# Kernel tuning notes

Hardware: AMD Instinct MI355X
Metric: run time of the kernel (lower is better)

The kernel has to match this reference:

```python
import jax, jax.numpy as jnp
import numpy as np

B, K, V, D, L = 16, 4, 32000, 512, 32   # batch, beam, vocab, d_model, max_decode_length
ALPHA, EOS = 0.6, 2
NEG_INF = 1.0e7   # matches inf('float32') in the torch source


def setup_inputs() -> dict:
    key = jax.random.key(0)
    k1, k2, k3, k4 = jax.random.split(key, 4)
    return {
        "initial_ids": jax.random.randint(k1, (B,), 0, V, dtype=jnp.int32),
        "init_cache_h": jax.random.normal(k2, (B, D), jnp.float32),
        "embed": jax.random.normal(k3, (V, D), jnp.float32) * 0.02,
        "proj": jax.random.normal(k4, (D, V), jnp.float32) * 0.02,
    }


def _beam_search(initial_ids, init_cache_h, embed, proj):
    # initial state (padded seq of length L+1; token 0 slot holds initial ids)
    alive_seq = jnp.zeros((B, K, L + 1), jnp.int32).at[:, :, 0].set(initial_ids[:, None])
    alive_lp = jnp.tile(jnp.array([[0.0] + [-NEG_INF] * (K - 1)], jnp.float32), (B, 1))
    cache_h = jnp.broadcast_to(init_cache_h[:, None, :], (B, K, D))
    fin_seq = jnp.zeros((B, K, L + 1), jnp.int32)
    fin_sc = jnp.full((B, K), -NEG_INF, jnp.float32)
    fin_fl = jnp.zeros((B, K), bool)

    def step(state, i):
        alive_seq, alive_lp, cache_h, fin_seq, fin_sc, fin_fl = state
        # symbols_to_logits_fn: tanh-RNN LM on the last emitted token
        last = alive_seq[:, :, i]                       # [B,K] traced index -> dynamic slice
        h = jnp.tanh(cache_h + embed[last])             # [B,K,D]
        logits = jnp.einsum('bkd,dv->bkv', h, proj)     # [B,K,V]
        # log-prob combine over flattened beam*vocab, keep 2K candidates
        lp = jax.nn.log_softmax(logits, axis=-1) + alive_lp[:, :, None]
        topk_lp, topk_idx = jax.lax.top_k(lp.reshape(B, K * V), 2 * K)
        beam_idx = topk_idx // V                        # [B,2K]
        ids = topk_idx % V
        # gather beams (seq + cache) and append new token at position i+1
        topk_seq = jnp.take_along_axis(alive_seq, beam_idx[:, :, None], axis=1)
        topk_seq = topk_seq.at[:, :, i + 1].set(ids)
        new_h = jnp.take_along_axis(h, beam_idx[:, :, None], axis=1)
        new_fl = ids == EOS                             # [B,2K]
        # new alive: penalize finished, keep top K
        alive_sc = topk_lp + new_fl.astype(jnp.float32) * -NEG_INF
        n_alive_lp, top_i = jax.lax.top_k(alive_sc, K)
        n_alive_seq = jnp.take_along_axis(topk_seq, top_i[:, :, None], axis=1)
        n_cache = jnp.take_along_axis(new_h, top_i[:, :, None], axis=1)
        # new finished: length-normalized scores, merge with previous finished
        ln = ((5.0 + (i + 1).astype(jnp.float32)) / 6.0) ** ALPHA
        new_scores = topk_lp / ln + (1.0 - new_fl.astype(jnp.float32)) * -NEG_INF
        comb_seq = jnp.concatenate([fin_seq, topk_seq], axis=1)   # [B,3K,L+1]
        comb_sc = jnp.concatenate([fin_sc, new_scores], axis=1)
        comb_fl = jnp.concatenate([fin_fl, new_fl], axis=1)
        n_fin_sc, top_fi = jax.lax.top_k(comb_sc, K)
        n_fin_seq = jnp.take_along_axis(comb_seq, top_fi[:, :, None], axis=1)
        n_fin_fl = jnp.take_along_axis(comb_fl, top_fi, axis=1)
        return (n_alive_seq, n_alive_lp, n_cache, n_fin_seq, n_fin_sc, n_fin_fl), None

    state0 = (alive_seq, alive_lp, cache_h, fin_seq, fin_sc, fin_fl)
    (alive_seq, alive_lp, _, fin_seq, fin_sc, fin_fl), _ = jax.lax.scan(
        step, state0, jnp.arange(L))
    # _process_finished_state: fall back to alive beams if nothing finished
    any_fin = jnp.any(fin_fl, axis=1)
    seq = jnp.where(any_fin[:, None, None], fin_seq.astype(jnp.float32),
                    alive_seq.astype(jnp.float32))
    sc = jnp.where(any_fin[:, None], fin_sc, alive_lp)
    return seq, sc


def reference(initial_ids, init_cache_h, embed, proj):
    return _beam_search(initial_ids, init_cache_h, embed, proj)
```

## Files before the change

kernel.cpp:

```cpp
#include <hip/hip_runtime.h>
#include <math.h>

#define BB 16
#define KK 4
#define VV 32000
#define DD 512
#define LL 32
#define EOS_ID 2
#define NEGINF 1.0e7f
#define ALPHA_C 0.6f
#define NROW (BB * KK)
#define NBLK 500
#define NSLOT 8
#define SPLIT_S 2048.0f

typedef _Float16 f16x8 __attribute__((ext_vector_type(8)));
typedef float f32x4 __attribute__((ext_vector_type(4)));

#define GLOAD_LDS16(gp, lp) \
    __builtin_amdgcn_global_load_lds( \
        (const __attribute__((address_space(1))) void*)(gp), \
        (__attribute__((address_space(3))) void*)(lp), 16, 0, 0)

#define INS8(v, idx, lv, li)                                          \
    if ((v) > lv[7]) {                                                \
        bool c_[8];                                                   \
        _Pragma("unroll")                                             \
        for (int j_ = 0; j_ < 8; j_++) c_[j_] = (v) > lv[j_];         \
        _Pragma("unroll")                                             \
        for (int j_ = 7; j_ >= 1; j_--) {                             \
            lv[j_] = c_[j_] ? (c_[j_ - 1] ? lv[j_ - 1] : (v)) : lv[j_];   \
            li[j_] = c_[j_] ? (c_[j_ - 1] ? li[j_ - 1] : (idx)) : li[j_]; \
        }                                                             \
        if (c_[0]) { lv[0] = (v); li[0] = (idx); }                    \
    }

__device__ inline void pack_h(int r, int d, float v,
                              _Float16* __restrict__ hfrag_hi,
                              _Float16* __restrict__ hfrag_lo) {
    _Float16 hi = (_Float16)v;
    _Float16 lo = (_Float16)((v - (float)hi) * SPLIT_S);
    int rg = r >> 4;
    int ks = d >> 5;
    int lane = (r & 15) + 16 * ((d >> 3) & 3);
    int e = d & 7;
    int off = (((rg * 16 + ks) * 64) + lane) * 8 + e;
    hfrag_hi[off] = hi;
    hfrag_lo[off] = lo;
}

__global__ void k_init(const int* __restrict__ initial_ids,
                       int* alive_seq, float* alive_lp,
                       int* fin_seq, float* fin_sc, int* fin_fl) {
    int tid = blockIdx.x * blockDim.x + threadIdx.x;
    int nthreads = gridDim.x * blockDim.x;
    const int SEQ = NROW * (LL + 1);
    for (int idx = tid; idx < SEQ; idx += nthreads) {
        int pos = idx % (LL + 1);
        int b = (idx / (LL + 1)) / KK;
        alive_seq[idx] = (pos == 0) ? initial_ids[b] : 0;
        fin_seq[idx] = 0;
    }
    for (int idx = tid; idx < NROW; idx += nthreads) {
        int k = idx % KK;
        alive_lp[idx] = (k == 0) ? 0.0f : -NEGINF;
        fin_sc[idx] = -NEGINF;
        fin_fl[idx] = 0;
    }
}

__global__ __launch_bounds__(256) void k_bconv(const float* __restrict__ proj,
                                               _Float16* __restrict__ bfrag_hi,
                                               _Float16* __restrict__ bfrag_lo) {
    int ct = blockIdx.x;
    int t = threadIdx.x;
    int w = t >> 6, l = t & 63;
    int col = ct * 16 + (l & 15);
    int kg = l >> 4;
    for (int ks = w; ks < 16; ks += 4) {
        int k0 = ks * 32 + kg * 8;
        f16x8 hi, lo;
        #pragma unroll
        for (int j = 0; j < 8; j++) {
            float v = proj[(size_t)(k0 + j) * VV + col];
            _Float16 h = (_Float16)v;
            hi[j] = h;
            lo[j] = (_Float16)((v - (float)h) * SPLIT_S);
        }
        size_t off = (size_t)(ct * 16 + ks) * 64 + l;
        reinterpret_cast<f16x8*>(bfrag_hi)[off] = hi;
        reinterpret_cast<f16x8*>(bfrag_lo)[off] = lo;
    }
}

__global__ void k_hinit(const int* __restrict__ initial_ids,
                        const float* __restrict__ init_h,
                        const float* __restrict__ embed,
                        float* __restrict__ h_buf,
                        _Float16* __restrict__ hfrag_hi,
                        _Float16* __restrict__ hfrag_lo) {
    int row = blockIdx.x;
    int b = row >> 2;
    int t = threadIdx.x;
    int tok = initial_ids[b];
    for (int d = t; d < DD; d += 256) {
        float v = tanhf(init_h[b * DD + d] + embed[(size_t)tok * DD + d]);
        h_buf[row * DD + d] = v;
        pack_h(row, d, v, hfrag_hi, hfrag_lo);
    }
}

__global__ __launch_bounds__(256) void k_logits(
        const _Float16* __restrict__ bfrag_hi,
        const _Float16* __restrict__ bfrag_lo,
        const _Float16* __restrict__ hfrag_hi,
        const _Float16* __restrict__ hfrag_lo,
        float* __restrict__ ptv, int* __restrict__ pti,
        float* __restrict__ pm, float* __restrict__ ps) {
    int t = threadIdx.x;
    int w = t >> 6, l = t & 63;
    int ct0 = blockIdx.x * 4;
    int c0 = ct0 * 16;
    int colr = l & 15;
    int kg = l >> 4;
    int lq = l * 8;

    __shared__ _Float16 Bs[NSLOT][4][2][512];

    f16x8 ah[16], al[16];
    #pragma unroll
    for (int ks = 0; ks < 16; ks++) {
        ah[ks] = *reinterpret_cast<const f16x8*>(hfrag_hi + ((w * 16 + ks) * 64 + l) * 8);
        al[ks] = *reinterpret_cast<const f16x8*>(hfrag_lo + ((w * 16 + ks) * 64 + l) * 8);
    }
    asm volatile("s_waitcnt vmcnt(0)" ::: "memory");
    __builtin_amdgcn_sched_barrier(0);

    f32x4 acc1[4], acc2[4];
    #pragma unroll
    for (int c2 = 0; c2 < 4; c2++) {
        acc1[c2] = (f32x4){0.f, 0.f, 0.f, 0.f};
        acc2[c2] = (f32x4){0.f, 0.f, 0.f, 0.f};
    }

    auto stage = [&](int s) {
        int slot = s & 7;
        const _Float16* gh = bfrag_hi + (((size_t)(ct0 + w) * 16 + s) * 64 + l) * 8;
        const _Float16* gl = bfrag_lo + (((size_t)(ct0 + w) * 16 + s) * 64 + l) * 8;
        GLOAD_LDS16(gh, &Bs[slot][w][0][0]);
        GLOAD_LDS16(gl, &Bs[slot][w][1][0]);
    };

    stage(0); stage(1); stage(2); stage(3); stage(4); stage(5); stage(6);

#define ITER(ks, NWAIT)                                                         \
    {                                                                           \
        asm volatile("s_waitcnt vmcnt(" #NWAIT ")" ::: "memory");               \
        __builtin_amdgcn_s_barrier();                                           \
        if ((ks) + 7 < 16) stage((ks) + 7);                                     \
        f16x8 bq[4][2];                                                         \
        _Pragma("unroll")                                                       \
        for (int c2 = 0; c2 < 4; c2++) {                                        \
            bq[c2][0] = *reinterpret_cast<const f16x8*>(&Bs[(ks) & 7][c2][0][lq]); \
            bq[c2][1] = *reinterpret_cast<const f16x8*>(&Bs[(ks) & 7][c2][1][lq]); \
        }                                                                       \
        asm volatile("s_waitcnt lgkmcnt(0)" ::: "memory");                      \
        _Pragma("unroll")                                                       \
        for (int c2 = 0; c2 < 4; c2++) {                                        \
            acc1[c2] = __builtin_amdgcn_mfma_f32_16x16x32_f16(ah[(ks)], bq[c2][0], acc1[c2], 0, 0, 0); \
            acc2[c2] = __builtin_amdgcn_mfma_f32_16x16x32_f16(ah[(ks)], bq[c2][1], acc2[c2], 0, 0, 0); \
            acc2[c2] = __builtin_amdgcn_mfma_f32_16x16x32_f16(al[(ks)], bq[c2][0], acc2[c2], 0, 0, 0); \
        }                                                                       \
    }

    ITER(0, 12)  ITER(1, 12)  ITER(2, 12)  ITER(3, 12)
    ITER(4, 12)  ITER(5, 12)  ITER(6, 12)  ITER(7, 12)
    ITER(8, 12)  ITER(9, 12)  ITER(10, 10) ITER(11, 8)
    ITER(12, 6)  ITER(13, 4)  ITER(14, 2)  ITER(15, 0)
#undef ITER

    char* pool = (char*)&Bs[0][0][0][0];
    float* Cs  = (float*)pool;
    float* sv  = (float*)(pool + 16640);
    int*   si  = (int*)  (pool + 24832);
    float* smx = (float*)(pool + 33024);
    float* ssm = (float*)(pool + 34048);

    #pragma unroll
    for (int c2 = 0; c2 < 4; c2++)
        #pragma unroll
        for (int j = 0; j < 4; j++)
            Cs[(w * 16 + kg * 4 + j) * 65 + c2 * 16 + colr] =
                acc1[c2][j] + acc2[c2][j] * (1.0f / SPLIT_S);
    __syncthreads();

    int row = t >> 2, cg = t & 3;
    float lv[8]; int li[8];
    #pragma unroll
    for (int j = 0; j < 8; j++) { lv[j] = -INFINITY; li[j] = 0x7fffffff; }
    float m = -INFINITY, s = 0.0f;
    #pragma unroll
    for (int cc = 0; cc < 16; cc++) {
        float v = Cs[row * 65 + cg * 16 + cc];
        int idx = c0 + cg * 16 + cc;
        float M = fmaxf(m, v);
        s = s * expf(m - M) + expf(v - M);
        m = M;
        INS8(v, idx, lv, li)
    }
    #pragma unroll
    for (int j = 0; j < 8; j++) { sv[t * 8 + j] = lv[j]; si[t * 8 + j] = li[j]; }
    smx[t] = m; ssm[t] = s;
    __syncthreads();
    for (int st = 2; st > 0; st >>= 1) {
        if ((t & 3) < st) {
            float rv[8]; int ri[8];
            int pa = 0, pb = 0;
            #pragma unroll
            for (int j = 0; j < 8; j++) {
                bool aok = pa < 8, bok = pb < 8;
                float va = sv[t * 8 + (aok ? pa : 7)], vb = sv[(t + st) * 8 + (bok ? pb : 7)];
                int   ia = si[t * 8 + (aok ? pa : 7)], ib = si[(t + st) * 8 + (bok ? pb : 7)];
                bool takeA = !bok || (aok && ((va > vb) || (va == vb && ia <= ib)));
                if (takeA) { rv[j] = va; ri[j] = ia; pa++; }
                else       { rv[j] = vb; ri[j] = ib; pb++; }
            }
            #pragma unroll
            for (int j = 0; j < 8; j++) { sv[t * 8 + j] = rv[j]; si[t * 8 + j] = ri[j]; }
            float ma = smx[t], mb = smx[t + st];
            float M = fmaxf(ma, mb);
            ssm[t] = ssm[t] * expf(ma - M) + ssm[t + st] * expf(mb - M);
            smx[t] = M;
        }
        __syncthreads();
    }
    if ((t & 3) == 0) {
        size_t base = ((size_t)row * NBLK + blockIdx.x) * 8;
        #pragma unroll
        for (int j = 0; j < 8; j++) { ptv[base + j] = sv[t * 8 + j]; pti[base + j] = si[t * 8 + j]; }
        pm[(size_t)row * NBLK + blockIdx.x] = smx[t];
        ps[(size_t)row * NBLK + blockIdx.x] = ssm[t];
    }
}

__global__ __launch_bounds__(256) void k_merge(
        const float* __restrict__ ptv, const int* __restrict__ pti,
        const float* __restrict__ pm, const float* __restrict__ ps,
        float* __restrict__ rowtop_val, int* __restrict__ rowtop_idx,
        float* __restrict__ row_lse) {
    int row = blockIdx.x, t = threadIdx.x;
    __shared__ float sval[256][8]; __shared__ int sidx[256][8];
    __shared__ float sm[256], ss[256];
    const float* pv = ptv + (size_t)row * NBLK * 8;
    const int*   pi = pti + (size_t)row * NBLK * 8;

    #pragma unroll
    for (int j = 0; j < 8; j++) { sval[t][j] = pv[t * 8 + j]; sidx[t][j] = pi[t * 8 + j]; }
    float m = pm[(size_t)row * NBLK + t], s = ps[(size_t)row * NBLK + t];
    if (t + 256 < NBLK) {
        const float* bv = pv + (size_t)(t + 256) * 8;
        const int*   bi = pi + (size_t)(t + 256) * 8;
        float rv[8]; int ri[8];
        int pa = 0, pb = 0;
        #pragma unroll
        for (int j = 0; j < 8; j++) {
            bool aok = pa < 8, bok = pb < 8;
            float va = sval[t][aok ? pa : 7], vb = bv[bok ? pb : 7];
            int   ia = sidx[t][aok ? pa : 7], ib = bi[bok ? pb : 7];
            bool takeA = !bok || (aok && ((va > vb) || (va == vb && ia <= ib)));
            if (takeA) { rv[j] = va; ri[j] = ia; pa++; }
            else       { rv[j] = vb; ri[j] = ib; pb++; }
        }
        #pragma unroll
        for (int j = 0; j < 8; j++) { sval[t][j] = rv[j]; sidx[t][j] = ri[j]; }
        float mb = pm[(size_t)row * NBLK + t + 256], sb = ps[(size_t)row * NBLK + t + 256];
        float M = fmaxf(m, mb);
        s = s * expf(m - M) + sb * expf(mb - M);
        m = M;
    }
    sm[t] = m; ss[t] = s;
    __syncthreads();
    for (int st = 128; st > 0; st >>= 1) {
        if (t < st) {
            float rv[8]; int ri[8];
            int pa = 0, pb = 0;
            #pragma unroll
            for (int j = 0; j < 8; j++) {
                bool aok = pa < 8, bok = pb < 8;
                float va = sval[t][aok ? pa : 7], vb = sval[t + st][bok ? pb : 7];
                int   ia = sidx[t][aok ? pa : 7], ib = sidx[t + st][bok ? pb : 7];
                bool takeA = !bok || (aok && ((va > vb) || (va == vb && ia <= ib)));
                if (takeA) { rv[j] = va; ri[j] = ia; pa++; }
                else       { rv[j] = vb; ri[j] = ib; pb++; }
            }
            #pragma unroll
            for (int j = 0; j < 8; j++) { sval[t][j] = rv[j]; sidx[t][j] = ri[j]; }
            float ma = sm[t], mb = sm[t + st];
            float M = fmaxf(ma, mb);
            ss[t] = ss[t] * expf(ma - M) + ss[t + st] * expf(mb - M);
            sm[t] = M;
        }
        __syncthreads();
    }
    if (t == 0) {
        #pragma unroll
        for (int j = 0; j < 8; j++) {
            rowtop_val[row * 8 + j] = sval[0][j];
            rowtop_idx[row * 8 + j] = sidx[0][j];
        }
        row_lse[row] = sm[0] + logf(ss[0]);
    }
}

__global__ __launch_bounds__(256) void k_update(
        const float* __restrict__ embed,
        float* h_buf, int* alive_seq, float* alive_lp,
        int* fin_seq, float* fin_sc, int* fin_fl,
        const float* __restrict__ rowtop_val, const int* __restrict__ rowtop_idx,
        const float* __restrict__ row_lse,
        _Float16* __restrict__ hfrag_hi, _Float16* __restrict__ hfrag_lo,
        int step) {
    int b = blockIdx.x;
    int t = threadIdx.x;
    __shared__ float h_old[KK][DD];
    __shared__ int old_aseq[KK][LL + 1], old_fseq[KK][LL + 1];
    __shared__ float lse_s[KK], alp_s[KK];
    __shared__ float clp[32]; __shared__ int cidx[32];
    __shared__ float c_lp[8];  __shared__ int c_beam[8], c_id[8], c_fl[8];
    __shared__ float asc_s[8], comb_s[12]; __shared__ int combfl_s[12];
    __shared__ int sel_alive[KK], sel_fin[KK];
    __shared__ float n_alp[KK], n_fsc[KK]; __shared__ int n_ffl[KK];

    for (int idx = t; idx < KK * (LL + 1); idx += 256) {
        old_aseq[idx / (LL + 1)][idx % (LL + 1)] = alive_seq[b * KK * (LL + 1) + idx];
        old_fseq[idx / (LL + 1)][idx % (LL + 1)] = fin_seq[b * KK * (LL + 1) + idx];
    }
    for (int idx = t; idx < KK * DD; idx += 256)
        h_old[idx >> 9][idx & (DD - 1)] = h_buf[b * KK * DD + idx];
    if (t < KK) {
        int r = b * KK + t;
        lse_s[t] = row_lse[r];
        alp_s[t] = alive_lp[r];
    }
    __syncthreads();

    if (t < 32) {
        int row = t >> 3;
        int src = (b * KK + row) * 8 + (t & 7);
        clp[t] = rowtop_val[src] - lse_s[row] + alp_s[row];
        cidx[t] = rowtop_idx[src];
    }
    __syncthreads();
    if (t < 32) {
        int row = t >> 3;
        float mylp = clp[t];
        int mykey = row * VV + cidx[t];
        int cnt = 0;
        #pragma unroll
        for (int j = 0; j < 32; j++) {
            int kj = (j >> 3) * VV + cidx[j];
            cnt += (clp[j] > mylp) || (clp[j] == mylp && kj < mykey);
        }
        if (cnt < 8) {
            c_lp[cnt] = mylp; c_beam[cnt] = row; c_id[cnt] = cidx[t];
            c_fl[cnt] = (cidx[t] == EOS_ID) ? 1 : 0;
        }
    }
    __syncthreads();
    if (t < 8) asc_s[t] = c_lp[t] + (c_fl[t] ? -NEGINF : 0.0f);
    if (t >= 64 && t < 76) {
        int j2 = t - 64;
        if (j2 < 4) { comb_s[j2] = fin_sc[b * KK + j2]; combfl_s[j2] = fin_fl[b * KK + j2]; }
        else {
            int cc = j2 - 4;
            float ln = powf((6.0f + (float)step) / 6.0f, ALPHA_C);
            comb_s[j2] = c_lp[cc] / ln + (c_fl[cc] ? 0.0f : -NEGINF);
            combfl_s[j2] = c_fl[cc];
        }
    }
    __syncthreads();
    if (t < 8) {
        float a = asc_s[t];
        int cnt = 0;
        #pragma unroll
        for (int j = 0; j < 8; j++) cnt += (asc_s[j] > a) || (asc_s[j] == a && j < t);
        if (cnt < KK) { sel_alive[cnt] = t; n_alp[cnt] = a; }
    }
    if (t >= 64 && t < 76) {
        int j2 = t - 64;
        float cval = comb_s[j2];
        int cnt = 0;
        #pragma unroll
        for (int j = 0; j < 12; j++) cnt += (comb_s[j] > cval) || (comb_s[j] == cval && j < j2);
        if (cnt < KK) { sel_fin[cnt] = j2; n_fsc[cnt] = cval; n_ffl[cnt] = combfl_s[j2]; }
    }
    __syncthreads();

    for (int idx = t; idx < KK * (LL + 1); idx += 256) {
        int j = idx / (LL + 1), p = idx % (LL + 1);
        int cand = sel_alive[j], bm = c_beam[cand];
        alive_seq[b * KK * (LL + 1) + idx] = (p == step + 1) ? c_id[cand] : old_aseq[bm][p];
        int src = sel_fin[j];
        int fval;
        if (src < 4) fval = old_fseq[src][p];
        else {
            int c2 = src - 4, bm2 = c_beam[c2];
            fval = (p == step + 1) ? c_id[c2] : old_aseq[bm2][p];
        }
        fin_seq[b * KK * (LL + 1) + idx] = fval;
    }
    for (int idx = t; idx < KK * DD; idx += 256) {
        int j = idx >> 9, d = idx & (DD - 1);
        int cand = sel_alive[j], bm = c_beam[cand], tok = c_id[cand];
        float v = tanhf(h_old[bm][d] + embed[(size_t)tok * DD + d]);
        int r = b * KK + j;
        h_buf[(size_t)r * DD + d] = v;
        pack_h(r, d, v, hfrag_hi, hfrag_lo);
    }
    if (t < KK) {
        alive_lp[b * KK + t] = n_alp[t];
        fin_sc[b * KK + t] = n_fsc[t];
        fin_fl[b * KK + t] = n_ffl[t];
    }
}

__global__ void k_final(const int* __restrict__ alive_seq, const float* __restrict__ alive_lp,
                        const int* __restrict__ fin_seq, const float* __restrict__ fin_sc,
                        const int* __restrict__ fin_fl, float* __restrict__ out) {
    int b = blockIdx.x;
    int t = threadIdx.x;
    __shared__ int anyf;
    if (t == 0)
        anyf = fin_fl[b * KK] | fin_fl[b * KK + 1] | fin_fl[b * KK + 2] | fin_fl[b * KK + 3];
    __syncthreads();
    for (int idx = t; idx < KK * (LL + 1); idx += blockDim.x) {
        int src = anyf ? fin_seq[b * KK * (LL + 1) + idx] : alive_seq[b * KK * (LL + 1) + idx];
        out[b * KK * (LL + 1) + idx] = (float)src;
    }
    if (t < KK)
        out[BB * KK * (LL + 1) + b * KK + t] = anyf ? fin_sc[b * KK + t] : alive_lp[b * KK + t];
}

extern "C" void kernel_launch(void* const* d_in, const int* in_sizes, int n_in,
                              void* d_out, int out_size, void* d_ws, size_t ws_size,
                              hipStream_t stream) {
    const int* initial_ids = (const int*)d_in[0];
    const float* init_h = (const float*)d_in[1];
    const float* embed = (const float*)d_in[2];
    const float* proj = (const float*)d_in[3];
    float* out = (float*)d_out;

    char* ws = (char*)d_ws;
    size_t off = 0;
    auto alloc = [&](size_t bytes) -> void* {
        off = (off + 255) & ~(size_t)255;
        void* p = ws + off;
        off += bytes;
        return p;
    };
    int* alive_seq    = (int*)alloc((size_t)NROW * (LL + 1) * 4);
    int* fin_seq      = (int*)alloc((size_t)NROW * (LL + 1) * 4);
    float* alive_lp   = (float*)alloc((size_t)NROW * 4);
    float* fin_sc     = (float*)alloc((size_t)NROW * 4);
    int* fin_fl       = (int*)alloc((size_t)NROW * 4);
    float* h_buf      = (float*)alloc((size_t)NROW * DD * 4);
    float* ptv        = (float*)alloc((size_t)NROW * NBLK * 8 * 4);
    int* pti          = (int*)alloc((size_t)NROW * NBLK * 8 * 4);
    float* pm         = (float*)alloc((size_t)NROW * NBLK * 4);
    float* ps         = (float*)alloc((size_t)NROW * NBLK * 4);
    float* rowtop_val = (float*)alloc((size_t)NROW * 8 * 4);
    int* rowtop_idx   = (int*)alloc((size_t)NROW * 8 * 4);
    float* row_lse    = (float*)alloc((size_t)NROW * 4);
    _Float16* hfrag_hi = (_Float16*)alloc((size_t)NROW * DD * 2);
    _Float16* hfrag_lo = (_Float16*)alloc((size_t)NROW * DD * 2);
    _Float16* bfrag_hi = (_Float16*)alloc((size_t)VV * DD * 2);
    _Float16* bfrag_lo = (_Float16*)alloc((size_t)VV * DD * 2);

    k_init<<<16, 256, 0, stream>>>(initial_ids, alive_seq, alive_lp,
                                   fin_seq, fin_sc, fin_fl);
    k_bconv<<<2000, 256, 0, stream>>>(proj, bfrag_hi, bfrag_lo);
    k_hinit<<<NROW, 256, 0, stream>>>(initial_ids, init_h, embed, h_buf,
                                      hfrag_hi, hfrag_lo);
    for (int step = 0; step < LL; step++) {
        k_logits<<<NBLK, 256, 0, stream>>>(bfrag_hi, bfrag_lo, hfrag_hi, hfrag_lo,
                                           ptv, pti, pm, ps);
        k_merge<<<NROW, 256, 0, stream>>>(ptv, pti, pm, ps,
                                          rowtop_val, rowtop_idx, row_lse);
        k_update<<<BB, 256, 0, stream>>>(embed, h_buf, alive_seq, alive_lp,
                                         fin_seq, fin_sc, fin_fl,
                                         rowtop_val, rowtop_idx, row_lse,
                                         hfrag_hi, hfrag_lo, step);
    }
    k_final<<<BB, 64, 0, stream>>>(alive_seq, alive_lp, fin_seq, fin_sc, fin_fl, out);
}
```

Measured before the change: 1.469 ms.

## Fuse per-step logits, merge and update into one persistent cooperative kernel

Replaces the 96 per-step kernel launches with a single cooperative persistent kernel that loops over decode steps. Grid-wide syncs separate the tiled logits/top-k phase from the merge and beam-update phase, which 16 blocks run. The LDS staging ring shrinks from 8 to 4 slots so two blocks fit per CU, and blocks loop over tiles when the grid is smaller than 500. This is meant to remove launch gaps between steps. In exchange it adds grid-sync cost, leaves most blocks idle during the serial update phase, and uses a shallower prefetch pipeline.

```diff
diff --git a/kernel.cpp b/kernel.cpp
--- a/kernel.cpp
+++ b/kernel.cpp
@@ -1,5 +1,8 @@
 #include <hip/hip_runtime.h>
+#include <hip/hip_cooperative_groups.h>
 #include <math.h>
+
+namespace cg = cooperative_groups;
 
 #define BB 16
 #define KK 4
@@ -11,7 +14,6 @@
 #define ALPHA_C 0.6f
 #define NROW (BB * KK)
 #define NBLK 500
-#define NSLOT 8
 #define SPLIT_S 2048.0f
 
 typedef _Float16 f16x8 __attribute__((ext_vector_type(8)));
@@ -110,7 +112,333 @@
     }
 }
 
-__global__ __launch_bounds__(256) void k_logits(
+__global__ __launch_bounds__(256, 2) void k_loop(
+        const _Float16* __restrict__ bfrag_hi,
+        const _Float16* __restrict__ bfrag_lo,
+        _Float16* __restrict__ hfrag_hi,
+        _Float16* __restrict__ hfrag_lo,
+        const float* __restrict__ embed,
+        float* h_buf, int* alive_seq, float* alive_lp,
+        int* fin_seq, float* fin_sc, int* fin_fl,
+        float* ptv, int* pti, float* pm, float* ps) {
+    cg::grid_group grid = cg::this_grid();
+    int t = threadIdx.x;
+    int w = t >> 6, l = t & 63;
+    int colr = l & 15;
+    int kg = l >> 4;
+    int lq = l * 8;
+
+    __shared__ _Float16 Bs[4][4][2][512];
+
+    for (int step = 0; step < LL; step++) {
+        {
+            f16x8 ah[16], al[16];
+            #pragma unroll
+            for (int ks = 0; ks < 16; ks++) {
+                ah[ks] = *reinterpret_cast<const f16x8*>(hfrag_hi + ((w * 16 + ks) * 64 + l) * 8);
+                al[ks] = *reinterpret_cast<const f16x8*>(hfrag_lo + ((w * 16 + ks) * 64 + l) * 8);
+            }
+
+            for (int tile = blockIdx.x; tile < NBLK; tile += gridDim.x) {
+                int ct0 = tile * 4;
+                int c0 = ct0 * 16;
+                asm volatile("s_waitcnt vmcnt(0)" ::: "memory");
+                __builtin_amdgcn_sched_barrier(0);
+
+                f32x4 acc1[4], acc2[4];
+                #pragma unroll
+                for (int c2 = 0; c2 < 4; c2++) {
+                    acc1[c2] = (f32x4){0.f, 0.f, 0.f, 0.f};
+                    acc2[c2] = (f32x4){0.f, 0.f, 0.f, 0.f};
+                }
+
+                auto stage = [&](int s) {
+                    int slot = s & 3;
+                    const _Float16* gh = bfrag_hi + (((size_t)(ct0 + w) * 16 + s) * 64 + l) * 8;
+                    const _Float16* gl = bfrag_lo + (((size_t)(ct0 + w) * 16 + s) * 64 + l) * 8;
+                    GLOAD_LDS16(gh, &Bs[slot][w][0][0]);
+                    GLOAD_LDS16(gl, &Bs[slot][w][1][0]);
+                };
+
+                stage(0); stage(1); stage(2);
+
+#define ITER(ks, NWAIT)                                                         \
+    {                                                                           \
+        asm volatile("s_waitcnt vmcnt(" #NWAIT ")" ::: "memory");               \
+        __builtin_amdgcn_s_barrier();                                           \
+        if ((ks) + 3 < 16) stage((ks) + 3);                                     \
+        f16x8 bq[4][2];                                                         \
+        _Pragma("unroll")                                                       \
+        for (int c2 = 0; c2 < 4; c2++) {                                        \
+            bq[c2][0] = *reinterpret_cast<const f16x8*>(&Bs[(ks) & 3][c2][0][lq]); \
+            bq[c2][1] = *reinterpret_cast<const f16x8*>(&Bs[(ks) & 3][c2][1][lq]); \
+        }                                                                       \
+        asm volatile("s_waitcnt lgkmcnt(0)" ::: "memory");                      \
+        _Pragma("unroll")                                                       \
+        for (int c2 = 0; c2 < 4; c2++) {                                        \
+            acc1[c2] = __builtin_amdgcn_mfma_f32_16x16x32_f16(ah[(ks)], bq[c2][0], acc1[c2], 0, 0, 0); \
+            acc2[c2] = __builtin_amdgcn_mfma_f32_16x16x32_f16(ah[(ks)], bq[c2][1], acc2[c2], 0, 0, 0); \
+            acc2[c2] = __builtin_amdgcn_mfma_f32_16x16x32_f16(al[(ks)], bq[c2][0], acc2[c2], 0, 0, 0); \
+        }                                                                       \
+    }
+
+                ITER(0, 4)  ITER(1, 4)  ITER(2, 4)  ITER(3, 4)
+                ITER(4, 4)  ITER(5, 4)  ITER(6, 4)  ITER(7, 4)
+                ITER(8, 4)  ITER(9, 4)  ITER(10, 4) ITER(11, 4)
+                ITER(12, 4) ITER(13, 4) ITER(14, 2) ITER(15, 0)
+#undef ITER
+
+                char* pool = (char*)&Bs[0][0][0][0];
+                float* Cs = (float*)pool;
+                #pragma unroll
+                for (int c2 = 0; c2 < 4; c2++)
+                    #pragma unroll
+                    for (int j = 0; j < 4; j++)
+                        Cs[(w * 16 + kg * 4 + j) * 65 + c2 * 16 + colr] =
+                            acc1[c2][j] + acc2[c2][j] * (1.0f / SPLIT_S);
+                __syncthreads();
+
+                int row = t >> 2, cg2 = t & 3;
+                float lv[8]; int li[8];
+                #pragma unroll
+                for (int j = 0; j < 8; j++) { lv[j] = -INFINITY; li[j] = 0x7fffffff; }
+                float m = -INFINITY, s = 0.0f;
+                #pragma unroll
+                for (int cc = 0; cc < 16; cc++) {
+                    float v = Cs[row * 65 + cg2 * 16 + cc];
+                    int idx = c0 + cg2 * 16 + cc;
+                    float M = fmaxf(m, v);
+                    s = s * expf(m - M) + expf(v - M);
+                    m = M;
+                    INS8(v, idx, lv, li)
+                }
+                __syncthreads();
+                float* sv  = (float*)pool;
+                int*   si  = (int*)  (pool + 8192);
+                float* smx = (float*)(pool + 16384);
+                float* ssm = (float*)(pool + 17408);
+                #pragma unroll
+                for (int j = 0; j < 8; j++) { sv[t * 8 + j] = lv[j]; si[t * 8 + j] = li[j]; }
+                smx[t] = m; ssm[t] = s;
+                __syncthreads();
+                for (int st = 2; st > 0; st >>= 1) {
+                    if ((t & 3) < st) {
+                        float rv[8]; int ri[8];
+                        int pa = 0, pb = 0;
+                        #pragma unroll
+                        for (int j = 0; j < 8; j++) {
+                            bool aok = pa < 8, bok = pb < 8;
+                            float va = sv[t * 8 + (aok ? pa : 7)], vb = sv[(t + st) * 8 + (bok ? pb : 7)];
+                            int   ia = si[t * 8 + (aok ? pa : 7)], ib = si[(t + st) * 8 + (bok ? pb : 7)];
+                            bool takeA = !bok || (aok && ((va > vb) || (va == vb && ia <= ib)));
+                            if (takeA) { rv[j] = va; ri[j] = ia; pa++; }
+                            else       { rv[j] = vb; ri[j] = ib; pb++; }
+                        }
+                        #pragma unroll
+                        for (int j = 0; j < 8; j++) { sv[t * 8 + j] = rv[j]; si[t * 8 + j] = ri[j]; }
+                        float ma = smx[t], mb = smx[t + st];
+                        float M = fmaxf(ma, mb);
+                        ssm[t] = ssm[t] * expf(ma - M) + ssm[t + st] * expf(mb - M);
+                        smx[t] = M;
+                    }
+                    __syncthreads();
+                }
+                if ((t & 3) == 0) {
+                    size_t base = ((size_t)row * NBLK + tile) * 8;
+                    #pragma unroll
+                    for (int j = 0; j < 8; j++) { ptv[base + j] = sv[t * 8 + j]; pti[base + j] = si[t * 8 + j]; }
+                    pm[(size_t)row * NBLK + tile] = smx[t];
+                    ps[(size_t)row * NBLK + tile] = ssm[t];
+                }
+                __syncthreads();
+            }
+        }
+        __threadfence();
+        grid.sync();
+
+        if (blockIdx.x < BB) {
+            int b = blockIdx.x;
+            int rloc = t >> 6, lane = t & 63;
+            int grow = b * KK + rloc;
+
+            char* pool = (char*)&Bs[0][0][0][0];
+            float* msv   = (float*)pool;
+            int*   msi   = (int*)  (pool + 9216);
+            float* msm   = (float*)(pool + 18432);
+            float* mss   = (float*)(pool + 19456);
+            float* h_old = (float*)(pool + 20480);
+            int* old_a   = (int*)  (pool + 28672);
+            int* old_f   = (int*)  (pool + 29248);
+            float* lse_s = (float*)(pool + 29824);
+            float* alp_s = (float*)(pool + 29840);
+            float* clp   = (float*)(pool + 29856);
+            int*   cidx  = (int*)  (pool + 29984);
+            float* c_lp  = (float*)(pool + 30112);
+            int* c_beam  = (int*)  (pool + 30144);
+            int* c_id    = (int*)  (pool + 30176);
+            int* c_fl    = (int*)  (pool + 30208);
+            float* asc_s = (float*)(pool + 30240);
+            float* comb_s= (float*)(pool + 30272);
+            int* combfl_s= (int*)  (pool + 30320);
+            int* sel_alive=(int*)  (pool + 30368);
+            int* sel_fin = (int*)  (pool + 30384);
+            float* n_alp = (float*)(pool + 30400);
+            float* n_fsc = (float*)(pool + 30416);
+            int* n_ffl   = (int*)  (pool + 30432);
+
+            for (int idx = t; idx < KK * (LL + 1); idx += 256) {
+                old_a[(idx / (LL + 1)) * 33 + idx % (LL + 1)] = alive_seq[b * KK * (LL + 1) + idx];
+                old_f[(idx / (LL + 1)) * 33 + idx % (LL + 1)] = fin_seq[b * KK * (LL + 1) + idx];
+            }
+            for (int idx = t; idx < KK * DD; idx += 256)
+                h_old[idx] = h_buf[b * KK * DD + idx];
+
+            float* Av = msv + (rloc * 64 + lane) * 9;
+            int*   Ai = msi + (rloc * 64 + lane) * 9;
+            const float* pv = ptv + (size_t)grow * NBLK * 8;
+            const int*   pi = pti + (size_t)grow * NBLK * 8;
+            #pragma unroll
+            for (int j = 0; j < 8; j++) { Av[j] = pv[lane * 8 + j]; Ai[j] = pi[lane * 8 + j]; }
+            float m = pm[(size_t)grow * NBLK + lane], s = ps[(size_t)grow * NBLK + lane];
+            for (int p = lane + 64; p < NBLK; p += 64) {
+                const float* bv = pv + (size_t)p * 8;
+                const int*   bi = pi + (size_t)p * 8;
+                float rv[8]; int ri[8];
+                int pa = 0, pb = 0;
+                #pragma unroll
+                for (int j = 0; j < 8; j++) {
+                    bool aok = pa < 8, bok = pb < 8;
+                    float va = Av[aok ? pa : 7], vb = bv[bok ? pb : 7];
+                    int   ia = Ai[aok ? pa : 7], ib = bi[bok ? pb : 7];
+                    bool takeA = !bok || (aok && ((va > vb) || (va == vb && ia <= ib)));
+                    if (takeA) { rv[j] = va; ri[j] = ia; pa++; }
+                    else       { rv[j] = vb; ri[j] = ib; pb++; }
+                }
+                #pragma unroll
+                for (int j = 0; j < 8; j++) { Av[j] = rv[j]; Ai[j] = ri[j]; }
+                float mb = pm[(size_t)grow * NBLK + p], sb = ps[(size_t)grow * NBLK + p];
+                float M = fmaxf(m, mb);
+                s = s * expf(m - M) + sb * expf(mb - M);
+                m = M;
+            }
+            msm[rloc * 64 + lane] = m; mss[rloc * 64 + lane] = s;
+            __syncthreads();
+            for (int st = 32; st > 0; st >>= 1) {
+                if (lane < st) {
+                    float* Bv2 = msv + (rloc * 64 + lane + st) * 9;
+                    int*   Bi2 = msi + (rloc * 64 + lane + st) * 9;
+                    float rv[8]; int ri[8];
+                    int pa = 0, pb = 0;
+                    #pragma unroll
+                    for (int j = 0; j < 8; j++) {
+                        bool aok = pa < 8, bok = pb < 8;
+                        float va = Av[aok ? pa : 7], vb = Bv2[bok ? pb : 7];
+                        int   ia = Ai[aok ? pa : 7], ib = Bi2[bok ? pb : 7];
+                        bool takeA = !bok || (aok && ((va > vb) || (va == vb && ia <= ib)));
+                        if (takeA) { rv[j] = va; ri[j] = ia; pa++; }
+                        else       { rv[j] = vb; ri[j] = ib; pb++; }
+                    }
+                    #pragma unroll
+                    for (int j = 0; j < 8; j++) { Av[j] = rv[j]; Ai[j] = ri[j]; }
+                    float ma = msm[rloc * 64 + lane], mb = msm[rloc * 64 + lane + st];
+                    float M = fmaxf(ma, mb);
+                    mss[rloc * 64 + lane] = mss[rloc * 64 + lane] * expf(ma - M)
+                                          + mss[rloc * 64 + lane + st] * expf(mb - M);
+                    msm[rloc * 64 + lane] = M;
+                }
+                __syncthreads();
+            }
+            if (t < KK) {
+                lse_s[t] = msm[t * 64] + logf(mss[t * 64]);
+                alp_s[t] = alive_lp[b * KK + t];
+            }
+            __syncthreads();
+
+            if (t < 32) {
+                int row = t >> 3;
+                clp[t] = msv[(row * 64) * 9 + (t & 7)] - lse_s[row] + alp_s[row];
+                cidx[t] = msi[(row * 64) * 9 + (t & 7)];
+            }
+            __syncthreads();
+            if (t < 32) {
+                int row = t >> 3;
+                float mylp = clp[t];
+                int mykey = row * VV + cidx[t];
+                int cnt = 0;
+                #pragma unroll
+                for (int j = 0; j < 32; j++) {
+                    int kj = (j >> 3) * VV + cidx[j];
+                    cnt += (clp[j] > mylp) || (clp[j] == mylp && kj < mykey);
+                }
+                if (cnt < 8) {
+                    c_lp[cnt] = mylp; c_beam[cnt] = row; c_id[cnt] = cidx[t];
+                    c_fl[cnt] = (cidx[t] == EOS_ID) ? 1 : 0;
+                }
+            }
+            __syncthreads();
+            if (t < 8) asc_s[t] = c_lp[t] + (c_fl[t] ? -NEGINF : 0.0f);
+            if (t >= 64 && t < 76) {
+                int j2 = t - 64;
+                if (j2 < 4) { comb_s[j2] = fin_sc[b * KK + j2]; combfl_s[j2] = fin_fl[b * KK + j2]; }
+                else {
+                    int cc = j2 - 4;
+                    float ln = powf((6.0f + (float)step) / 6.0f, ALPHA_C);
+                    comb_s[j2] = c_lp[cc] / ln + (c_fl[cc] ? 0.0f : -NEGINF);
+                    combfl_s[j2] = c_fl[cc];
+                }
+            }
+            __syncthreads();
+            if (t < 8) {
+                float a = asc_s[t];
+                int cnt = 0;
+                #pragma unroll
+                for (int j = 0; j < 8; j++) cnt += (asc_s[j] > a) || (asc_s[j] == a && j < t);
+                if (cnt < KK) { sel_alive[cnt] = t; n_alp[cnt] = a; }
+            }
+            if (t >= 64 && t < 76) {
+                int j2 = t - 64;
+                float cval = comb_s[j2];
+                int cnt = 0;
+                #pragma unroll
+                for (int j = 0; j < 12; j++) cnt += (comb_s[j] > cval) || (comb_s[j] == cval && j < j2);
+                if (cnt < KK) { sel_fin[cnt] = j2; n_fsc[cnt] = cval; n_ffl[cnt] = combfl_s[j2]; }
+            }
+            __syncthreads();
+
+            for (int idx = t; idx < KK * (LL + 1); idx += 256) {
+                int j = idx / (LL + 1), p = idx % (LL + 1);
+                int cand = sel_alive[j], bm = c_beam[cand];
+                alive_seq[b * KK * (LL + 1) + idx] = (p == step + 1) ? c_id[cand] : old_a[bm * 33 + p];
+                int src = sel_fin[j];
+                int fval;
+                if (src < 4) fval = old_f[src * 33 + p];
+                else {
+                    int c2 = src - 4, bm2 = c_beam[c2];
+                    fval = (p == step + 1) ? c_id[c2] : old_a[bm2 * 33 + p];
+                }
+                fin_seq[b * KK * (LL + 1) + idx] = fval;
+            }
+            for (int idx = t; idx < KK * DD; idx += 256) {
+                int j = idx >> 9, d = idx & (DD - 1);
+                int cand = sel_alive[j], bm = c_beam[cand], tok = c_id[cand];
+                float v = tanhf(h_old[bm * DD + d] + embed[(size_t)tok * DD + d]);
+                int r = b * KK + j;
+                h_buf[(size_t)r * DD + d] = v;
+                pack_h(r, d, v, hfrag_hi, hfrag_lo);
+            }
+            if (t < KK) {
+                alive_lp[b * KK + t] = n_alp[t];
+                fin_sc[b * KK + t] = n_fsc[t];
+                fin_fl[b * KK + t] = n_ffl[t];
+            }
+        }
+        __threadfence();
+        grid.sync();
+    }
+}
+
+#define NSLOT_FB 8
+__global__ __launch_bounds__(256) void k_logits_fb(
         const _Float16* __restrict__ bfrag_hi,
         const _Float16* __restrict__ bfrag_lo,
         const _Float16* __restrict__ hfrag_hi,
@@ -125,7 +453,7 @@
     int kg = l >> 4;
     int lq = l * 8;
 
-    __shared__ _Float16 Bs[NSLOT][4][2][512];
+    __shared__ _Float16 Bs[NSLOT_FB][4][2][512];
 
     f16x8 ah[16], al[16];
     #pragma unroll
@@ -153,7 +481,7 @@
 
     stage(0); stage(1); stage(2); stage(3); stage(4); stage(5); stage(6);
 
-#define ITER(ks, NWAIT)                                                         \
+#define ITERF(ks, NWAIT)                                                        \
     {                                                                           \
         asm volatile("s_waitcnt vmcnt(" #NWAIT ")" ::: "memory");               \
         __builtin_amdgcn_s_barrier();                                           \
@@ -173,11 +501,11 @@
         }                                                                       \
     }
 
-    ITER(0, 12)  ITER(1, 12)  ITER(2, 12)  ITER(3, 12)
-    ITER(4, 12)  ITER(5, 12)  ITER(6, 12)  ITER(7, 12)
-    ITER(8, 12)  ITER(9, 12)  ITER(10, 10) ITER(11, 8)
-    ITER(12, 6)  ITER(13, 4)  ITER(14, 2)  ITER(15, 0)
-#undef ITER
+    ITERF(0, 12)  ITERF(1, 12)  ITERF(2, 12)  ITERF(3, 12)
+    ITERF(4, 12)  ITERF(5, 12)  ITERF(6, 12)  ITERF(7, 12)
+    ITERF(8, 12)  ITERF(9, 12)  ITERF(10, 10) ITERF(11, 8)
+    ITERF(12, 6)  ITERF(13, 4)  ITERF(14, 2)  ITERF(15, 0)
+#undef ITERF
 
     char* pool = (char*)&Bs[0][0][0][0];
     float* Cs  = (float*)pool;
@@ -194,15 +522,15 @@
                 acc1[c2][j] + acc2[c2][j] * (1.0f / SPLIT_S);
     __syncthreads();
 
-    int row = t >> 2, cg = t & 3;
+    int row = t >> 2, cg2 = t & 3;
     float lv[8]; int li[8];
     #pragma unroll
     for (int j = 0; j < 8; j++) { lv[j] = -INFINITY; li[j] = 0x7fffffff; }
     float m = -INFINITY, s = 0.0f;
     #pragma unroll
     for (int cc = 0; cc < 16; cc++) {
-        float v = Cs[row * 65 + cg * 16 + cc];
-        int idx = c0 + cg * 16 + cc;
+        float v = Cs[row * 65 + cg2 * 16 + cc];
+        int idx = c0 + cg2 * 16 + cc;
         float M = fmaxf(m, v);
         s = s * expf(m - M) + expf(v - M);
         m = M;
@@ -481,15 +809,43 @@
     k_bconv<<<2000, 256, 0, stream>>>(proj, bfrag_hi, bfrag_lo);
     k_hinit<<<NROW, 256, 0, stream>>>(initial_ids, init_h, embed, h_buf,
                                       hfrag_hi, hfrag_lo);
-    for (int step = 0; step < LL; step++) {
-        k_logits<<<NBLK, 256, 0, stream>>>(bfrag_hi, bfrag_lo, hfrag_hi, hfrag_lo,
-                                           ptv, pti, pm, ps);
-        k_merge<<<NROW, 256, 0, stream>>>(ptv, pti, pm, ps,
-                                          rowtop_val, rowtop_idx, row_lse);
-        k_update<<<BB, 256, 0, stream>>>(embed, h_buf, alive_seq, alive_lp,
-                                         fin_seq, fin_sc, fin_fl,
-                                         rowtop_val, rowtop_idx, row_lse,
-                                         hfrag_hi, hfrag_lo, step);
+
+    int nbPerCU = 0;
+    hipError_t qrc = hipOccupancyMaxActiveBlocksPerMultiprocessor(&nbPerCU, k_loop, 256, 0);
+    int nCU = 256;
+    {
+        int dev = 0;
+        hipGetDevice(&dev);
+        hipDeviceProp_t prop;
+        if (hipGetDeviceProperties(&prop, dev) == hipSuccess && prop.multiProcessorCount > 0)
+            nCU = prop.multiProcessorCount;
+    }
+    int coopGrid = nbPerCU * nCU;
+    if (coopGrid > NBLK) coopGrid = NBLK;
+    bool useCoop = (qrc == hipSuccess) && (coopGrid >= BB);
+
+    if (useCoop) {
+        void* args[] = {
+            (void*)&bfrag_hi, (void*)&bfrag_lo, (void*)&hfrag_hi, (void*)&hfrag_lo,
+            (void*)&embed, (void*)&h_buf, (void*)&alive_seq, (void*)&alive_lp,
+            (void*)&fin_seq, (void*)&fin_sc, (void*)&fin_fl,
+            (void*)&ptv, (void*)&pti, (void*)&pm, (void*)&ps
+        };
+        hipError_t rc = hipLaunchCooperativeKernel((void*)k_loop, dim3(coopGrid), dim3(256),
+                                                   args, 0, stream);
+        if (rc != hipSuccess) useCoop = false;
+    }
+    if (!useCoop) {
+        for (int step = 0; step < LL; step++) {
+            k_logits_fb<<<NBLK, 256, 0, stream>>>(bfrag_hi, bfrag_lo, hfrag_hi, hfrag_lo,
+                                                  ptv, pti, pm, ps);
+            k_merge<<<NROW, 256, 0, stream>>>(ptv, pti, pm, ps,
+                                              rowtop_val, rowtop_idx, row_lse);
+            k_update<<<BB, 256, 0, stream>>>(embed, h_buf, alive_seq, alive_lp,
+                                             fin_seq, fin_sc, fin_fl,
+                                             rowtop_val, rowtop_idx, row_lse,
+                                             hfrag_hi, hfrag_lo, step);
+        }
     }
     k_final<<<BB, 64, 0, stream>>>(alive_seq, alive_lp, fin_seq, fin_sc, fin_fl, out);
 }
```

New measurement: 5.345 ms. 264% more time.

## Fuse beam update and hidden-state recompute into logits kernel prologue

Applied to the files above, without the earlier changes.

Removes the per-step k_update launch by folding the beam selection of the previous step into the prologue of the logits kernel. Every block redundantly recomputes the top-k candidate selection for all batches and rebuilds its MFMA A fragments directly from h_old and the embedding with tanh. The first 16 blocks also write the sequences, scores and the new h. Hidden state and alive log-probs are double-buffered so blocks can read the old state while others write the new one. This saves one launch and one pre-packed h buffer round trip per step, but adds redundant selection work and extra global reads to all 500 blocks.

```diff
diff --git a/kernel.cpp b/kernel.cpp
--- a/kernel.cpp
+++ b/kernel.cpp
@@ -35,20 +35,6 @@
         if (c_[0]) { lv[0] = (v); li[0] = (idx); }                    \
     }
 
-__device__ inline void pack_h(int r, int d, float v,
-                              _Float16* __restrict__ hfrag_hi,
-                              _Float16* __restrict__ hfrag_lo) {
-    _Float16 hi = (_Float16)v;
-    _Float16 lo = (_Float16)((v - (float)hi) * SPLIT_S);
-    int rg = r >> 4;
-    int ks = d >> 5;
-    int lane = (r & 15) + 16 * ((d >> 3) & 3);
-    int e = d & 7;
-    int off = (((rg * 16 + ks) * 64) + lane) * 8 + e;
-    hfrag_hi[off] = hi;
-    hfrag_lo[off] = lo;
-}
-
 __global__ void k_init(const int* __restrict__ initial_ids,
                        int* alive_seq, float* alive_lp,
                        int* fin_seq, float* fin_sc, int* fin_fl) {
@@ -96,27 +82,26 @@
 __global__ void k_hinit(const int* __restrict__ initial_ids,
                         const float* __restrict__ init_h,
                         const float* __restrict__ embed,
-                        float* __restrict__ h_buf,
-                        _Float16* __restrict__ hfrag_hi,
-                        _Float16* __restrict__ hfrag_lo) {
+                        float* __restrict__ h_buf) {
     int row = blockIdx.x;
     int b = row >> 2;
     int t = threadIdx.x;
     int tok = initial_ids[b];
-    for (int d = t; d < DD; d += 256) {
-        float v = tanhf(init_h[b * DD + d] + embed[(size_t)tok * DD + d]);
-        h_buf[row * DD + d] = v;
-        pack_h(row, d, v, hfrag_hi, hfrag_lo);
-    }
-}
-
-__global__ __launch_bounds__(256) void k_logits(
+    for (int d = t; d < DD; d += 256)
+        h_buf[row * DD + d] = tanhf(init_h[b * DD + d] + embed[(size_t)tok * DD + d]);
+}
+
+__global__ __launch_bounds__(256) void k_logits_fused(
         const _Float16* __restrict__ bfrag_hi,
         const _Float16* __restrict__ bfrag_lo,
-        const _Float16* __restrict__ hfrag_hi,
-        const _Float16* __restrict__ hfrag_lo,
+        const float* __restrict__ h_old, float* __restrict__ h_new,
+        const float* __restrict__ embed,
+        int* alive_seq, int* fin_seq, float* fin_sc, int* fin_fl,
+        const float* __restrict__ alive_lp_old, float* __restrict__ alive_lp_new,
+        const float* __restrict__ rowtop_val, const int* __restrict__ rowtop_idx,
+        const float* __restrict__ row_lse,
         float* __restrict__ ptv, int* __restrict__ pti,
-        float* __restrict__ pm, float* __restrict__ ps) {
+        float* __restrict__ pm, float* __restrict__ ps, int step) {
     int t = threadIdx.x;
     int w = t >> 6, l = t & 63;
     int ct0 = blockIdx.x * 4;
@@ -124,15 +109,181 @@
     int colr = l & 15;
     int kg = l >> 4;
     int lq = l * 8;
+    int trans = step - 1;
 
     __shared__ _Float16 Bs[NSLOT][4][2][512];
+    char* pool = (char*)&Bs[0][0][0][0];
 
     f16x8 ah[16], al[16];
-    #pragma unroll
-    for (int ks = 0; ks < 16; ks++) {
-        ah[ks] = *reinterpret_cast<const f16x8*>(hfrag_hi + ((w * 16 + ks) * 64 + l) * 8);
-        al[ks] = *reinterpret_cast<const f16x8*>(hfrag_lo + ((w * 16 + ks) * 64 + l) * 8);
-    }
+
+    if (step == 0) {
+        int r = w * 16 + (l & 15);
+        const float* hsrc = h_old + (size_t)r * DD;
+        #pragma unroll
+        for (int ks = 0; ks < 16; ks++) {
+            int d0 = ks * 32 + kg * 8;
+            float4 a4 = *reinterpret_cast<const float4*>(hsrc + d0);
+            float4 b4 = *reinterpret_cast<const float4*>(hsrc + d0 + 4);
+            float vv[8] = {a4.x, a4.y, a4.z, a4.w, b4.x, b4.y, b4.z, b4.w};
+            f16x8 hi8, lo8;
+            #pragma unroll
+            for (int e = 0; e < 8; e++) {
+                _Float16 h = (_Float16)vv[e];
+                hi8[e] = h;
+                lo8[e] = (_Float16)((vv[e] - (float)h) * SPLIT_S);
+            }
+            ah[ks] = hi8; al[ks] = lo8;
+        }
+    } else {
+        float* s_rtv   = (float*)pool;
+        int*   s_rti   = (int*)  (pool + 2048);
+        float* s_lse   = (float*)(pool + 4096);
+        float* s_alp   = (float*)(pool + 4352);
+        float* s_c     = (float*)(pool + 4608);
+        int*   s_ck    = (int*)  (pool + 6656);
+        float* s_clp2  = (float*)(pool + 8704);
+        int*   s_cbeam = (int*)  (pool + 9216);
+        int*   s_cid   = (int*)  (pool + 9728);
+        int*   s_bmrow = (int*)  (pool + 10240);
+        int*   s_tok   = (int*)  (pool + 10496);
+        float* s_nalp  = (float*)(pool + 10752);
+        int*   old_a   = (int*)  (pool + 11008);
+        int*   old_f   = (int*)  (pool + 11552);
+        float* comb    = (float*)(pool + 12096);
+        int*   combfl  = (int*)  (pool + 12160);
+        int*   selfin  = (int*)  (pool + 12224);
+        float* nfsc    = (float*)(pool + 12256);
+        int*   nffl    = (int*)  (pool + 12288);
+
+        for (int i = t; i < 512; i += 256) { s_rtv[i] = rowtop_val[i]; s_rti[i] = rowtop_idx[i]; }
+        if (t < 64) { s_lse[t] = row_lse[t]; s_alp[t] = alive_lp_old[t]; }
+        if (blockIdx.x < BB) {
+            int b = blockIdx.x;
+            for (int idx = t; idx < KK * (LL + 1); idx += 256) {
+                old_a[(idx / (LL + 1)) * 33 + idx % (LL + 1)] = alive_seq[b * KK * (LL + 1) + idx];
+                old_f[(idx / (LL + 1)) * 33 + idx % (LL + 1)] = fin_seq[b * KK * (LL + 1) + idx];
+            }
+        }
+        __syncthreads();
+        #pragma unroll
+        for (int p = 0; p < 2; p++) {
+            int batch = (t >> 5) + p * 8, c = t & 31;
+            int row = c >> 3, j = c & 7, gr = batch * 4 + row;
+            s_c[batch * 32 + c] = s_rtv[gr * 8 + j] - s_lse[gr] + s_alp[gr];
+            s_ck[batch * 32 + c] = row * VV + s_rti[gr * 8 + j];
+        }
+        __syncthreads();
+        #pragma unroll
+        for (int p = 0; p < 2; p++) {
+            int batch = (t >> 5) + p * 8, c = t & 31;
+            float my = s_c[batch * 32 + c];
+            int myk = s_ck[batch * 32 + c];
+            int cnt = 0;
+            #pragma unroll
+            for (int j = 0; j < 32; j++) {
+                float lj = s_c[batch * 32 + j];
+                int kj = s_ck[batch * 32 + j];
+                cnt += (lj > my) || (lj == my && kj < myk);
+            }
+            if (cnt < 8) {
+                s_cbeam[batch * 8 + cnt] = myk / VV;
+                s_cid[batch * 8 + cnt] = myk % VV;
+                s_clp2[batch * 8 + cnt] = my;
+            }
+        }
+        __syncthreads();
+        if (t < 128) {
+            int batch = t >> 3, c = t & 7;
+            float a = s_clp2[batch * 8 + c] + ((s_cid[batch * 8 + c] == EOS_ID) ? -NEGINF : 0.0f);
+            int cnt = 0;
+            #pragma unroll
+            for (int j = 0; j < 8; j++) {
+                float aj = s_clp2[batch * 8 + j] + ((s_cid[batch * 8 + j] == EOS_ID) ? -NEGINF : 0.0f);
+                cnt += (aj > a) || (aj == a && j < c);
+            }
+            if (cnt < KK) {
+                s_bmrow[batch * 4 + cnt] = batch * 4 + s_cbeam[batch * 8 + c];
+                s_tok[batch * 4 + cnt] = s_cid[batch * 8 + c];
+                s_nalp[batch * 4 + cnt] = a;
+            }
+        }
+        __syncthreads();
+
+        if (blockIdx.x < BB) {
+            int b = blockIdx.x;
+            if (t < 12) {
+                if (t < 4) { comb[t] = fin_sc[b * KK + t]; combfl[t] = fin_fl[b * KK + t]; }
+                else {
+                    int cc = t - 4;
+                    float ln = powf((6.0f + (float)trans) / 6.0f, ALPHA_C);
+                    int fl = (s_cid[b * 8 + cc] == EOS_ID) ? 1 : 0;
+                    comb[t] = s_clp2[b * 8 + cc] / ln + (fl ? 0.0f : -NEGINF);
+                    combfl[t] = fl;
+                }
+            }
+            __syncthreads();
+            if (t < 12) {
+                float cval = comb[t];
+                int cnt = 0;
+                #pragma unroll
+                for (int j = 0; j < 12; j++) cnt += (comb[j] > cval) || (comb[j] == cval && j < t);
+                if (cnt < KK) { selfin[cnt] = t; nfsc[cnt] = cval; nffl[cnt] = combfl[t]; }
+            }
+            __syncthreads();
+            for (int idx = t; idx < KK * (LL + 1); idx += 256) {
+                int j = idx / (LL + 1), p = idx % (LL + 1);
+                int bml = s_bmrow[b * 4 + j] - b * 4;
+                alive_seq[b * KK * (LL + 1) + idx] =
+                    (p == trans + 1) ? s_tok[b * 4 + j] : old_a[bml * 33 + p];
+                int src = selfin[j];
+                int fval;
+                if (src < 4) fval = old_f[src * 33 + p];
+                else {
+                    int c2 = src - 4, bm2 = s_cbeam[b * 8 + c2];
+                    fval = (p == trans + 1) ? s_cid[b * 8 + c2] : old_a[bm2 * 33 + p];
+                }
+                fin_seq[b * KK * (LL + 1) + idx] = fval;
+            }
+            for (int idx = t; idx < KK * DD; idx += 256) {
+                int j = idx >> 9, d = idx & (DD - 1);
+                int gr = b * 4 + j;
+                h_new[(size_t)gr * DD + d] =
+                    tanhf(h_old[(size_t)s_bmrow[gr] * DD + d] +
+                          embed[(size_t)s_tok[gr] * DD + d]);
+            }
+            if (t < KK) {
+                alive_lp_new[b * KK + t] = s_nalp[b * 4 + t];
+                fin_sc[b * KK + t] = nfsc[t];
+                fin_fl[b * KK + t] = nffl[t];
+            }
+        }
+
+        int r = w * 16 + (l & 15);
+        const float* hsrc = h_old + (size_t)s_bmrow[r] * DD;
+        const float* esrc = embed + (size_t)s_tok[r] * DD;
+        #pragma unroll
+        for (int ks = 0; ks < 16; ks++) {
+            int d0 = ks * 32 + kg * 8;
+            float4 a4 = *reinterpret_cast<const float4*>(hsrc + d0);
+            float4 b4 = *reinterpret_cast<const float4*>(hsrc + d0 + 4);
+            float4 ea = *reinterpret_cast<const float4*>(esrc + d0);
+            float4 eb = *reinterpret_cast<const float4*>(esrc + d0 + 4);
+            float vv[8] = {tanhf(a4.x + ea.x), tanhf(a4.y + ea.y),
+                           tanhf(a4.z + ea.z), tanhf(a4.w + ea.w),
+                           tanhf(b4.x + eb.x), tanhf(b4.y + eb.y),
+                           tanhf(b4.z + eb.z), tanhf(b4.w + eb.w)};
+            f16x8 hi8, lo8;
+            #pragma unroll
+            for (int e = 0; e < 8; e++) {
+                _Float16 h = (_Float16)vv[e];
+                hi8[e] = h;
+                lo8[e] = (_Float16)((vv[e] - (float)h) * SPLIT_S);
+            }
+            ah[ks] = hi8; al[ks] = lo8;
+        }
+        __syncthreads();
+    }
+
     asm volatile("s_waitcnt vmcnt(0)" ::: "memory");
     __builtin_amdgcn_sched_barrier(0);
 
@@ -179,7 +330,6 @@
     ITER(12, 6)  ITER(13, 4)  ITER(14, 2)  ITER(15, 0)
 #undef ITER
 
-    char* pool = (char*)&Bs[0][0][0][0];
     float* Cs  = (float*)pool;
     float* sv  = (float*)(pool + 16640);
     int*   si  = (int*)  (pool + 24832);
@@ -313,16 +463,13 @@
 }
 
 __global__ __launch_bounds__(256) void k_update(
-        const float* __restrict__ embed,
-        float* h_buf, int* alive_seq, float* alive_lp,
+        int* alive_seq, const float* __restrict__ alive_lp_old,
+        float* __restrict__ alive_lp_new,
         int* fin_seq, float* fin_sc, int* fin_fl,
         const float* __restrict__ rowtop_val, const int* __restrict__ rowtop_idx,
-        const float* __restrict__ row_lse,
-        _Float16* __restrict__ hfrag_hi, _Float16* __restrict__ hfrag_lo,
-        int step) {
+        const float* __restrict__ row_lse, int step) {
     int b = blockIdx.x;
     int t = threadIdx.x;
-    __shared__ float h_old[KK][DD];
     __shared__ int old_aseq[KK][LL + 1], old_fseq[KK][LL + 1];
     __shared__ float lse_s[KK], alp_s[KK];
     __shared__ float clp[32]; __shared__ int cidx[32];
@@ -335,12 +482,10 @@
         old_aseq[idx / (LL + 1)][idx % (LL + 1)] = alive_seq[b * KK * (LL + 1) + idx];
         old_fseq[idx / (LL + 1)][idx % (LL + 1)] = fin_seq[b * KK * (LL + 1) + idx];
     }
-    for (int idx = t; idx < KK * DD; idx += 256)
-        h_old[idx >> 9][idx & (DD - 1)] = h_buf[b * KK * DD + idx];
     if (t < KK) {
         int r = b * KK + t;
         lse_s[t] = row_lse[r];
-        alp_s[t] = alive_lp[r];
+        alp_s[t] = alive_lp_old[r];
     }
     __syncthreads();
 
@@ -409,16 +554,8 @@
         }
         fin_seq[b * KK * (LL + 1) + idx] = fval;
     }
-    for (int idx = t; idx < KK * DD; idx += 256) {
-        int j = idx >> 9, d = idx & (DD - 1);
-        int cand = sel_alive[j], bm = c_beam[cand], tok = c_id[cand];
-        float v = tanhf(h_old[bm][d] + embed[(size_t)tok * DD + d]);
-        int r = b * KK + j;
-        h_buf[(size_t)r * DD + d] = v;
-        pack_h(r, d, v, hfrag_hi, hfrag_lo);
-    }
     if (t < KK) {
-        alive_lp[b * KK + t] = n_alp[t];
+        alive_lp_new[b * KK + t] = n_alp[t];
         fin_sc[b * KK + t] = n_fsc[t];
         fin_fl[b * KK + t] = n_ffl[t];
     }
@@ -460,10 +597,12 @@
     };
     int* alive_seq    = (int*)alloc((size_t)NROW * (LL + 1) * 4);
     int* fin_seq      = (int*)alloc((size_t)NROW * (LL + 1) * 4);
-    float* alive_lp   = (float*)alloc((size_t)NROW * 4);
+    float* alpA       = (float*)alloc((size_t)NROW * 4);
+    float* alpB       = (float*)alloc((size_t)NROW * 4);
     float* fin_sc     = (float*)alloc((size_t)NROW * 4);
     int* fin_fl       = (int*)alloc((size_t)NROW * 4);
-    float* h_buf      = (float*)alloc((size_t)NROW * DD * 4);
+    float* hA         = (float*)alloc((size_t)NROW * DD * 4);
+    float* hB         = (float*)alloc((size_t)NROW * DD * 4);
     float* ptv        = (float*)alloc((size_t)NROW * NBLK * 8 * 4);
     int* pti          = (int*)alloc((size_t)NROW * NBLK * 8 * 4);
     float* pm         = (float*)alloc((size_t)NROW * NBLK * 4);
@@ -471,25 +610,29 @@
     float* rowtop_val = (float*)alloc((size_t)NROW * 8 * 4);
     int* rowtop_idx   = (int*)alloc((size_t)NROW * 8 * 4);
     float* row_lse    = (float*)alloc((size_t)NROW * 4);
-    _Float16* hfrag_hi = (_Float16*)alloc((size_t)NROW * DD * 2);
-    _Float16* hfrag_lo = (_Float16*)alloc((size_t)NROW * DD * 2);
     _Float16* bfrag_hi = (_Float16*)alloc((size_t)VV * DD * 2);
     _Float16* bfrag_lo = (_Float16*)alloc((size_t)VV * DD * 2);
 
-    k_init<<<16, 256, 0, stream>>>(initial_ids, alive_seq, alive_lp,
+    k_init<<<16, 256, 0, stream>>>(initial_ids, alive_seq, alpA,
                                    fin_seq, fin_sc, fin_fl);
     k_bconv<<<2000, 256, 0, stream>>>(proj, bfrag_hi, bfrag_lo);
-    k_hinit<<<NROW, 256, 0, stream>>>(initial_ids, init_h, embed, h_buf,
-                                      hfrag_hi, hfrag_lo);
-    for (int step = 0; step < LL; step++) {
-        k_logits<<<NBLK, 256, 0, stream>>>(bfrag_hi, bfrag_lo, hfrag_hi, hfrag_lo,
-                                           ptv, pti, pm, ps);
+    k_hinit<<<NROW, 256, 0, stream>>>(initial_ids, init_h, embed, hA);
+
+    for (int s = 0; s < LL; s++) {
+        const float* h_old = (s == 0) ? hA : (((s - 1) & 1) ? hB : hA);
+        float* h_new = (s & 1) ? hB : hA;
+        const float* alp_old = (s == 0) ? alpA : (((s - 1) & 1) ? alpB : alpA);
+        float* alp_new = (s & 1) ? alpB : alpA;
+        k_logits_fused<<<NBLK, 256, 0, stream>>>(
+            bfrag_hi, bfrag_lo, h_old, h_new, embed,
+            alive_seq, fin_seq, fin_sc, fin_fl,
+            alp_old, alp_new, rowtop_val, rowtop_idx, row_lse,
+            ptv, pti, pm, ps, s);
         k_merge<<<NROW, 256, 0, stream>>>(ptv, pti, pm, ps,
                                           rowtop_val, rowtop_idx, row_lse);
-        k_update<<<BB, 256, 0, stream>>>(embed, h_buf, alive_seq, alive_lp,
-                                         fin_seq, fin_sc, fin_fl,
-                                         rowtop_val, rowtop_idx, row_lse,
-                                         hfrag_hi, hfrag_lo, step);
-    }
-    k_final<<<BB, 64, 0, stream>>>(alive_seq, alive_lp, fin_seq, fin_sc, fin_fl, out);
-}
+    }
+    k_update<<<BB, 256, 0, stream>>>(alive_seq, alpB, alpA,
+                                     fin_seq, fin_sc, fin_fl,
+                                     rowtop_val, rowtop_idx, row_lse, LL - 1);
+    k_final<<<BB, 64, 0, stream>>>(alive_seq, alpA, fin_seq, fin_sc, fin_fl, out);
+}
```

Measured after the change: 2.434 ms. 1.66x slower.
